# Performance work log

Measured on AMD Instinct MI355X. Metric: run time of the kernel, lower is better.

The kernel has to match this reference:

```python
import jax, jax.numpy as jnp
import numpy as np

N_NODES = 50000
N_EDGES = 800000
NFEAT, NHID, NCLASS = 256, 128, 47


def _gcn_norm(edge_index, edge_weight, n):
    """PyG GCNConv normalization: add self-loops (weight 1) then symmetric deg^-1/2."""
    src, dst = edge_index[0], edge_index[1]
    loop = jnp.arange(n, dtype=src.dtype)
    src_f = jnp.concatenate([src, loop])
    dst_f = jnp.concatenate([dst, loop])
    w_f = jnp.concatenate([edge_weight, jnp.ones((n,), edge_weight.dtype)])
    deg = jax.ops.segment_sum(w_f, dst_f, num_segments=n)  # [n]
    deg_safe = jnp.where(deg > 0, deg, 1.0)
    dinv = jnp.where(deg > 0, jax.lax.rsqrt(deg_safe), 0.0)
    norm = dinv[src_f] * w_f * dinv[dst_f]  # [E + n]
    return src_f, dst_f, norm


def _gcn_conv(h, src, dst, norm, b, n):
    # gather transformed source features, scale, scatter-add into targets
    msg = h[src] * norm[:, None]  # [E+n, d]
    return jax.ops.segment_sum(msg, dst, num_segments=n) + b


def setup_inputs() -> dict:
    key = jax.random.key(0)
    k = jax.random.split(key, 8)
    x = jax.random.normal(k[0], (N_NODES, NFEAT), dtype=jnp.float32)
    edge_index = jax.random.randint(k[1], (2, N_EDGES), 0, N_NODES, dtype=jnp.int32)
    edge_weight = jax.random.uniform(k[2], (N_EDGES,), dtype=jnp.float32)
    W1 = jax.random.normal(k[3], (NFEAT, NHID), dtype=jnp.float32) * (1.0 / np.sqrt(NFEAT))
    b1 = jnp.zeros((NHID,), dtype=jnp.float32)
    W2 = jax.random.normal(k[4], (NHID, NCLASS), dtype=jnp.float32) * (1.0 / np.sqrt(NHID))
    b2 = jnp.zeros((NCLASS,), dtype=jnp.float32)
    return {"x": x, "edge_index": edge_index, "edge_weight": edge_weight,
            "W1": W1, "b1": b1, "W2": W2, "b2": b2}


def reference(x, edge_index, edge_weight, W1, b1, W2, b2):
    n = x.shape[0]
    src, dst, norm = _gcn_norm(edge_index, edge_weight, n)
    h = _gcn_conv(x @ W1, src, dst, norm, b1, n)   # GCNConv 1
    h = jax.nn.relu(h)                             # dropout is identity in eval
    h = _gcn_conv(h @ W2, src, dst, norm, b2, n)   # GCNConv 2
    return jax.nn.log_softmax(h, axis=1)
```

## Files before the change

kernel.cpp:

```cpp
#include <hip/hip_runtime.h>

#define N_NODES 50000
#define N_EDGES 800000
#define NFEAT   256
#define NHID    128
#define NCLASS  47
#define H2P     48
#define CSR_MAX (N_EDGES + 7 * N_NODES)
#define NSUB    8
#define G1_BLOCKS ((N_NODES + 63) / 64)

typedef __attribute__((ext_vector_type(8))) short short8v;
typedef __attribute__((ext_vector_type(4))) float f32x4;

__device__ __forceinline__ ushort f2bf(float f) {
    unsigned u = __float_as_uint(f);
    unsigned r = (u + 0x7FFF + ((u >> 16) & 1)) >> 16;
    return (ushort)r;
}
__device__ __forceinline__ float blo(unsigned u) { return __uint_as_float(u << 16); }
__device__ __forceinline__ float bhi(unsigned u) { return __uint_as_float(u & 0xFFFF0000u); }


__global__ void init_kernel(unsigned long long* __restrict__ packed,
                            int* __restrict__ total,
                            const float* __restrict__ W1, const float* __restrict__ W2,
                            ushort* __restrict__ w1t, ushort* __restrict__ w2t) {
    int t = blockIdx.x * blockDim.x + threadIdx.x;
    if (t < N_NODES * NSUB) packed[t] = 0ull;
    if (t == 0) *total = 0;
    if (t < NFEAT * NHID) {
        int k = t >> 7, c = t & 127;
        w1t[c * NFEAT + k] = f2bf(W1[(size_t)k * NHID + c]);
    }
    if (t < NHID * H2P) {
        int k = t / H2P, c = t % H2P;
        w2t[c * NHID + k] = (c < NCLASS) ? f2bf(W2[(size_t)k * NCLASS + c]) : 0;
    }
}


__global__ __launch_bounds__(256) void fused_gemm1_degcnt_kernel(
        const float* __restrict__ x, const ushort* __restrict__ w1t,
        ushort* __restrict__ h1b,
        const int* __restrict__ dst, const float* __restrict__ w,
        unsigned long long* __restrict__ packed, int* __restrict__ pos) {
    __shared__ __align__(16) ushort xs[64][72];
    __shared__ __align__(16) ushort ws[128][72];
    int tid = threadIdx.x;
    if (blockIdx.x >= G1_BLOCKS) {
        int e = (blockIdx.x - G1_BLOCKS) * 256 + tid;
        if (e < N_EDGES) {
            int d = dst[e];
            int b = e & (NSUB - 1);
            unsigned fx = __float2uint_rn(w[e] * 1048576.0f);
            unsigned long long old = atomicAdd(&packed[(size_t)b * N_NODES + d],
                                               (1ull << 40) | (unsigned long long)fx);
            pos[e] = (int)(old >> 40);
        }
        return;
    }
    int node0 = blockIdx.x * 64;
    int wave = tid >> 6, l = tid & 63;
    int fr = l & 15, fq = l >> 4;
    int r0 = (wave >> 1) * 32;
    int c0 = (wave & 1) * 64;

    f32x4 acc[2][4] = {};

    for (int kk0 = 0; kk0 < NFEAT; kk0 += 64) {
        {
            int row = tid >> 2, q = tid & 3;
            int srow = node0 + row; if (srow >= N_NODES) srow = N_NODES - 1;
            const float4* src = (const float4*)(x + (size_t)srow * NFEAT + kk0 + q * 16);
            ushort tmp[16];
            #pragma unroll
            for (int i = 0; i < 4; ++i) {
                float4 v = src[i];
                tmp[i * 4 + 0] = f2bf(v.x); tmp[i * 4 + 1] = f2bf(v.y);
                tmp[i * 4 + 2] = f2bf(v.z); tmp[i * 4 + 3] = f2bf(v.w);
            }
            #pragma unroll
            for (int i = 0; i < 2; ++i)
                *(short8v*)&xs[row][q * 16 + i * 8] = *(short8v*)&tmp[i * 8];
        }
        {
            int rr = tid >> 3;
            int cq = tid & 7;
            #pragma unroll
            for (int i = 0; i < 4; ++i) {
                int row = rr + i * 32;
                *(short8v*)&ws[row][cq * 8] =
                    *(const short8v*)&w1t[(size_t)row * NFEAT + kk0 + cq * 8];
            }
        }
        __syncthreads();
        short8v a[2][2], b[4][2];
        #pragma unroll
        for (int m = 0; m < 2; ++m)
            #pragma unroll
            for (int kf = 0; kf < 2; ++kf)
                a[m][kf] = *(const short8v*)&xs[r0 + m * 16 + fr][kf * 32 + fq * 8];
        #pragma unroll
        for (int n = 0; n < 4; ++n)
            #pragma unroll
            for (int kf = 0; kf < 2; ++kf)
                b[n][kf] = *(const short8v*)&ws[c0 + n * 16 + fr][kf * 32 + fq * 8];
        #pragma unroll
        for (int m = 0; m < 2; ++m)
            #pragma unroll
            for (int n = 0; n < 4; ++n)
                #pragma unroll
                for (int kf = 0; kf < 2; ++kf)
                    acc[m][n] = __builtin_amdgcn_mfma_f32_16x16x32_bf16(
                        a[m][kf], b[n][kf], acc[m][n], 0, 0, 0);
        __syncthreads();
    }
    #pragma unroll
    for (int m = 0; m < 2; ++m) {
        #pragma unroll
        for (int n = 0; n < 4; ++n) {
            #pragma unroll
            for (int j = 0; j < 4; ++j) {
                int gr = node0 + r0 + m * 16 + fq * 4 + j;
                if (gr < N_NODES)
                    h1b[(size_t)gr * NHID + c0 + n * 16 + fr] = f2bf(acc[m][n][j]);
            }
        }
    }
}

__global__ __launch_bounds__(256) void segalloc_kernel(const unsigned long long* __restrict__ packed,
                                                       int* __restrict__ counts,
                                                       float* __restrict__ dinv,
                                                       int* __restrict__ row_start,
                                                       int* __restrict__ sub_base,
                                                       int* __restrict__ total,
                                                       int2* __restrict__ csr, int n) {
    __shared__ int s[256];
    __shared__ int base_s;
    int t = threadIdx.x;
    int i = blockIdx.x * 256 + t;
    int v = 0, cnt = 0;
    if (i < n) {
        unsigned long long ws = 0;
        int sb[NSUB];
        #pragma unroll
        for (int b = 0; b < NSUB; ++b) {
            unsigned long long pk = packed[(size_t)b * N_NODES + i];
            sb[b] = cnt;
            cnt += (int)(pk >> 40);
            ws += (pk & 0xFFFFFFFFFFull);
        }
        counts[i] = cnt;
        float deg = 1.0f + (float)ws * (1.0f / 1048576.0f);
        dinv[i] = rsqrtf(deg);
        #pragma unroll
        for (int b = 0; b < NSUB; b += 4)
            *(int4*)&sub_base[(size_t)i * NSUB + b] = make_int4(sb[b], sb[b+1], sb[b+2], sb[b+3]);
        v = (cnt + 7) & ~7;
    }
    s[t] = v;
    __syncthreads();
    #pragma unroll
    for (int off = 1; off < 256; off <<= 1) {
        int x = s[t];
        if (t >= off) x += s[t - off];
        __syncthreads();
        s[t] = x;
        __syncthreads();
    }
    if (t == 255) base_s = atomicAdd(total, s[255]);
    __syncthreads();
    if (i < n) {
        int base = base_s + s[t] - v;
        row_start[i] = base;
        for (int k = cnt; k < v; ++k) csr[base + k] = make_int2(0, 0);
    }
}

__global__ void scatter_kernel(const int* __restrict__ src, const int* __restrict__ dst,
                               const float* __restrict__ w, const int* __restrict__ pos,
                               const float* __restrict__ dinv,
                               const int* __restrict__ row_start,
                               const int* __restrict__ sub_base,
                               int2* __restrict__ csr, int E) {
    int e = blockIdx.x * blockDim.x + threadIdx.x;
    if (e >= E) return;
    int d = dst[e], s = src[e];
    int b = e & (NSUB - 1);
    int p = row_start[d] + sub_base[(size_t)d * NSUB + b] + pos[e];
    int2 pr;
    pr.x = s;
    pr.y = __float_as_int(dinv[s] * w[e] * dinv[d]);
    csr[p] = pr;
}


__global__ __launch_bounds__(256) void agg1_kernel(const ushort* __restrict__ h1b,
                                                   const int* __restrict__ row_start,
                                                   const int* __restrict__ counts,
                                                   const int2* __restrict__ csr,
                                                   const float* __restrict__ dinv,
                                                   const float* __restrict__ b1,
                                                   ushort* __restrict__ haggb) {
    int wv = threadIdx.x >> 6;
    int i = blockIdx.x * 4 + wv;
    int l = threadIdx.x & 63;
    int h = l >> 5, q = l & 31;
    const ushort* rowp = h1b + 4 * q;

    float di = dinv[i];
    float sc = (h == 0) ? di * di : 0.f;
    uint2 sv = *(const uint2*)(rowp + (size_t)i * NHID);
    float4 acc;
    acc.x = sc * blo(sv.x); acc.y = sc * bhi(sv.x);
    acc.z = sc * blo(sv.y); acc.w = sc * bhi(sv.y);

    int lo = row_start[i], hi = lo + ((counts[i] + 7) & ~7);
    int e = lo;
    for (; e + 16 <= hi; e += 16) {
        int2 pA = csr[e + 0 + h],  pB = csr[e + 2 + h];
        int2 pC = csr[e + 4 + h],  pD = csr[e + 6 + h];
        int2 pE = csr[e + 8 + h],  pF = csr[e + 10 + h];
        int2 pG = csr[e + 12 + h], pH = csr[e + 14 + h];
        uint2 vA = *(const uint2*)(rowp + (size_t)pA.x * NHID);
        uint2 vB = *(const uint2*)(rowp + (size_t)pB.x * NHID);
        uint2 vC = *(const uint2*)(rowp + (size_t)pC.x * NHID);
        uint2 vD = *(const uint2*)(rowp + (size_t)pD.x * NHID);
        uint2 vE = *(const uint2*)(rowp + (size_t)pE.x * NHID);
        uint2 vF = *(const uint2*)(rowp + (size_t)pF.x * NHID);
        uint2 vG = *(const uint2*)(rowp + (size_t)pG.x * NHID);
        uint2 vH = *(const uint2*)(rowp + (size_t)pH.x * NHID);
        float wA = __int_as_float(pA.y), wB = __int_as_float(pB.y);
        float wC = __int_as_float(pC.y), wD = __int_as_float(pD.y);
        float wE = __int_as_float(pE.y), wF = __int_as_float(pF.y);
        float wG = __int_as_float(pG.y), wH = __int_as_float(pH.y);
        acc.x = fmaf(wA, blo(vA.x), acc.x); acc.y = fmaf(wA, bhi(vA.x), acc.y);
        acc.z = fmaf(wA, blo(vA.y), acc.z); acc.w = fmaf(wA, bhi(vA.y), acc.w);
        acc.x = fmaf(wB, blo(vB.x), acc.x); acc.y = fmaf(wB, bhi(vB.x), acc.y);
        acc.z = fmaf(wB, blo(vB.y), acc.z); acc.w = fmaf(wB, bhi(vB.y), acc.w);
        acc.x = fmaf(wC, blo(vC.x), acc.x); acc.y = fmaf(wC, bhi(vC.x), acc.y);
        acc.z = fmaf(wC, blo(vC.y), acc.z); acc.w = fmaf(wC, bhi(vC.y), acc.w);
        acc.x = fmaf(wD, blo(vD.x), acc.x); acc.y = fmaf(wD, bhi(vD.x), acc.y);
        acc.z = fmaf(wD, blo(vD.y), acc.z); acc.w = fmaf(wD, bhi(vD.y), acc.w);
        acc.x = fmaf(wE, blo(vE.x), acc.x); acc.y = fmaf(wE, bhi(vE.x), acc.y);
        acc.z = fmaf(wE, blo(vE.y), acc.z); acc.w = fmaf(wE, bhi(vE.y), acc.w);
        acc.x = fmaf(wF, blo(vF.x), acc.x); acc.y = fmaf(wF, bhi(vF.x), acc.y);
        acc.z = fmaf(wF, blo(vF.y), acc.z); acc.w = fmaf(wF, bhi(vF.y), acc.w);
        acc.x = fmaf(wG, blo(vG.x), acc.x); acc.y = fmaf(wG, bhi(vG.x), acc.y);
        acc.z = fmaf(wG, blo(vG.y), acc.z); acc.w = fmaf(wG, bhi(vG.y), acc.w);
        acc.x = fmaf(wH, blo(vH.x), acc.x); acc.y = fmaf(wH, bhi(vH.x), acc.y);
        acc.z = fmaf(wH, blo(vH.y), acc.z); acc.w = fmaf(wH, bhi(vH.y), acc.w);
    }
    if (e < hi) {
        int2 pA = csr[e + 0 + h], pB = csr[e + 2 + h];
        int2 pC = csr[e + 4 + h], pD = csr[e + 6 + h];
        uint2 vA = *(const uint2*)(rowp + (size_t)pA.x * NHID);
        uint2 vB = *(const uint2*)(rowp + (size_t)pB.x * NHID);
        uint2 vC = *(const uint2*)(rowp + (size_t)pC.x * NHID);
        uint2 vD = *(const uint2*)(rowp + (size_t)pD.x * NHID);
        float wA = __int_as_float(pA.y), wB = __int_as_float(pB.y);
        float wC = __int_as_float(pC.y), wD = __int_as_float(pD.y);
        acc.x = fmaf(wA, blo(vA.x), acc.x); acc.y = fmaf(wA, bhi(vA.x), acc.y);
        acc.z = fmaf(wA, blo(vA.y), acc.z); acc.w = fmaf(wA, bhi(vA.y), acc.w);
        acc.x = fmaf(wB, blo(vB.x), acc.x); acc.y = fmaf(wB, bhi(vB.x), acc.y);
        acc.z = fmaf(wB, blo(vB.y), acc.z); acc.w = fmaf(wB, bhi(vB.y), acc.w);
        acc.x = fmaf(wC, blo(vC.x), acc.x); acc.y = fmaf(wC, bhi(vC.x), acc.y);
        acc.z = fmaf(wC, blo(vC.y), acc.z); acc.w = fmaf(wC, bhi(vC.y), acc.w);
        acc.x = fmaf(wD, blo(vD.x), acc.x); acc.y = fmaf(wD, bhi(vD.x), acc.y);
        acc.z = fmaf(wD, blo(vD.y), acc.z); acc.w = fmaf(wD, bhi(vD.y), acc.w);
    }
    acc.x += __shfl_xor(acc.x, 32);
    acc.y += __shfl_xor(acc.y, 32);
    acc.z += __shfl_xor(acc.z, 32);
    acc.w += __shfl_xor(acc.w, 32);
    if (h == 0) {
        float4 bb = *(const float4*)(b1 + 4 * q);
        acc.x = fmaxf(acc.x + bb.x, 0.f);
        acc.y = fmaxf(acc.y + bb.y, 0.f);
        acc.z = fmaxf(acc.z + bb.z, 0.f);
        acc.w = fmaxf(acc.w + bb.w, 0.f);
        uint2 o;
        o.x = (unsigned)f2bf(acc.x) | ((unsigned)f2bf(acc.y) << 16);
        o.y = (unsigned)f2bf(acc.z) | ((unsigned)f2bf(acc.w) << 16);
        *(uint2*)(haggb + (size_t)i * NHID + 4 * q) = o;
    }
}


__global__ __launch_bounds__(256) void gemm2_kernel(const ushort* __restrict__ haggb,
                                                    const ushort* __restrict__ w2t,
                                                    ushort* __restrict__ h2b) {
    __shared__ __align__(16) ushort ha[64][136];
    __shared__ __align__(16) ushort wt[48][136];
    int tid = threadIdx.x;
    int node0 = blockIdx.x * 64;
    {
        int row = tid >> 2, q = tid & 3;
        int srow = node0 + row; if (srow >= N_NODES) srow = N_NODES - 1;
        const short8v* src = (const short8v*)(haggb + (size_t)srow * NHID + q * 32);
        #pragma unroll
        for (int i = 0; i < 4; ++i)
            *(short8v*)&ha[row][q * 32 + i * 8] = src[i];
    }
    {
        #pragma unroll
        for (int i = 0; i < 3; ++i) {
            int id = tid + i * 256;
            int row = id >> 4, cq = id & 15;
            *(short8v*)&wt[row][cq * 8] =
                *(const short8v*)&w2t[(size_t)row * NHID + cq * 8];
        }
    }
    __syncthreads();
    int wave = tid >> 6, l = tid & 63;
    int fr = l & 15, fq = l >> 4;
    int r0 = wave * 16;
    short8v a[4], b[3][4];
    #pragma unroll
    for (int kf = 0; kf < 4; ++kf)
        a[kf] = *(const short8v*)&ha[r0 + fr][kf * 32 + fq * 8];
    #pragma unroll
    for (int n = 0; n < 3; ++n)
        #pragma unroll
        for (int kf = 0; kf < 4; ++kf)
            b[n][kf] = *(const short8v*)&wt[n * 16 + fr][kf * 32 + fq * 8];
    f32x4 acc[3] = {};
    #pragma unroll
    for (int n = 0; n < 3; ++n)
        #pragma unroll
        for (int kf = 0; kf < 4; ++kf)
            acc[n] = __builtin_amdgcn_mfma_f32_16x16x32_bf16(a[kf], b[n][kf], acc[n], 0, 0, 0);
    #pragma unroll
    for (int n = 0; n < 3; ++n) {
        #pragma unroll
        for (int j = 0; j < 4; ++j) {
            int gr = node0 + r0 + fq * 4 + j;
            int col = n * 16 + fr;
            if (gr < N_NODES && col < H2P)
                h2b[(size_t)gr * H2P + col] = (col < NCLASS) ? f2bf(acc[n][j]) : 0;
        }
    }
}


__global__ __launch_bounds__(256) void agg2_kernel(const ushort* __restrict__ h2b,
                                                   const int* __restrict__ row_start,
                                                   const int* __restrict__ counts,
                                                   const int2* __restrict__ csr,
                                                   const float* __restrict__ dinv,
                                                   const float* __restrict__ b2,
                                                   float* __restrict__ out, int n) {
    int wv = threadIdx.x >> 6;
    int i = blockIdx.x * 4 + wv;
    if (i >= n) return;
    int l = threadIdx.x & 63;
    int h = l >> 5, q = l & 31;
    bool act = q < 24;
    int qq = act ? q : 0;
    const ushort* rowp = h2b + 2 * qq;

    float di = dinv[i];
    float sc = (h == 0 && act) ? di * di : 0.f;
    unsigned sv = *(const unsigned*)(rowp + (size_t)i * H2P);
    float2 acc;
    acc.x = sc * blo(sv); acc.y = sc * bhi(sv);

    int lo = row_start[i], hi = lo + ((counts[i] + 7) & ~7);
    int e = lo;
    for (; e + 16 <= hi; e += 16) {
        int2 pA = csr[e + 0 + h],  pB = csr[e + 2 + h];
        int2 pC = csr[e + 4 + h],  pD = csr[e + 6 + h];
        int2 pE = csr[e + 8 + h],  pF = csr[e + 10 + h];
        int2 pG = csr[e + 12 + h], pH = csr[e + 14 + h];
        unsigned vA = *(const unsigned*)(rowp + (size_t)pA.x * H2P);
        unsigned vB = *(const unsigned*)(rowp + (size_t)pB.x * H2P);
        unsigned vC = *(const unsigned*)(rowp + (size_t)pC.x * H2P);
        unsigned vD = *(const unsigned*)(rowp + (size_t)pD.x * H2P);
        unsigned vE = *(const unsigned*)(rowp + (size_t)pE.x * H2P);
        unsigned vF = *(const unsigned*)(rowp + (size_t)pF.x * H2P);
        unsigned vG = *(const unsigned*)(rowp + (size_t)pG.x * H2P);
        unsigned vH = *(const unsigned*)(rowp + (size_t)pH.x * H2P);
        float wA = __int_as_float(pA.y), wB = __int_as_float(pB.y);
        float wC = __int_as_float(pC.y), wD = __int_as_float(pD.y);
        float wE = __int_as_float(pE.y), wF = __int_as_float(pF.y);
        float wG = __int_as_float(pG.y), wH = __int_as_float(pH.y);
        acc.x = fmaf(wA, blo(vA), acc.x); acc.y = fmaf(wA, bhi(vA), acc.y);
        acc.x = fmaf(wB, blo(vB), acc.x); acc.y = fmaf(wB, bhi(vB), acc.y);
        acc.x = fmaf(wC, blo(vC), acc.x); acc.y = fmaf(wC, bhi(vC), acc.y);
        acc.x = fmaf(wD, blo(vD), acc.x); acc.y = fmaf(wD, bhi(vD), acc.y);
        acc.x = fmaf(wE, blo(vE), acc.x); acc.y = fmaf(wE, bhi(vE), acc.y);
        acc.x = fmaf(wF, blo(vF), acc.x); acc.y = fmaf(wF, bhi(vF), acc.y);
        acc.x = fmaf(wG, blo(vG), acc.x); acc.y = fmaf(wG, bhi(vG), acc.y);
        acc.x = fmaf(wH, blo(vH), acc.x); acc.y = fmaf(wH, bhi(vH), acc.y);
    }
    if (e < hi) {
        int2 pA = csr[e + 0 + h], pB = csr[e + 2 + h];
        int2 pC = csr[e + 4 + h], pD = csr[e + 6 + h];
        unsigned vA = *(const unsigned*)(rowp + (size_t)pA.x * H2P);
        unsigned vB = *(const unsigned*)(rowp + (size_t)pB.x * H2P);
        unsigned vC = *(const unsigned*)(rowp + (size_t)pC.x * H2P);
        unsigned vD = *(const unsigned*)(rowp + (size_t)pD.x * H2P);
        float wA = __int_as_float(pA.y), wB = __int_as_float(pB.y);
        float wC = __int_as_float(pC.y), wD = __int_as_float(pD.y);
        acc.x = fmaf(wA, blo(vA), acc.x); acc.y = fmaf(wA, bhi(vA), acc.y);
        acc.x = fmaf(wB, blo(vB), acc.x); acc.y = fmaf(wB, bhi(vB), acc.y);
        acc.x = fmaf(wC, blo(vC), acc.x); acc.y = fmaf(wC, bhi(vC), acc.y);
        acc.x = fmaf(wD, blo(vD), acc.x); acc.y = fmaf(wD, bhi(vD), acc.y);
    }
    acc.x += __shfl_xor(acc.x, 32);
    acc.y += __shfl_xor(acc.y, 32);

    float v0 = -1e30f, v1 = -1e30f;
    if (act) {
        v0 = acc.x + b2[2 * q];
        v1 = (2 * q + 1 < NCLASS) ? (acc.y + b2[2 * q + 1]) : -1e30f;
    }
    float pm = fmaxf(v0, v1);
    #pragma unroll
    for (int off = 16; off; off >>= 1) pm = fmaxf(pm, __shfl_xor(pm, off));
    float ex = 0.f;
    if (act) {
        ex = __expf(v0 - pm);
        if (2 * q + 1 < NCLASS) ex += __expf(v1 - pm);
    }
    #pragma unroll
    for (int off = 16; off; off >>= 1) ex += __shfl_xor(ex, off);
    if (h == 0 && act) {
        float ls = pm + __logf(ex);
        out[(size_t)i * NCLASS + 2 * q] = v0 - ls;
        if (2 * q + 1 < NCLASS) out[(size_t)i * NCLASS + 2 * q + 1] = v1 - ls;
    }
}


extern "C" void kernel_launch(void* const* d_in, const int* in_sizes, int n_in,
                              void* d_out, int out_size, void* d_ws, size_t ws_size,
                              hipStream_t stream) {
    const float* x  = (const float*)d_in[0];
    const int*   ei = (const int*)d_in[1];
    const float* ew = (const float*)d_in[2];
    const float* W1 = (const float*)d_in[3];
    const float* b1 = (const float*)d_in[4];
    const float* W2 = (const float*)d_in[5];
    const float* b2 = (const float*)d_in[6];
    float* out = (float*)d_out;

    const int* e_src = ei;
    const int* e_dst = ei + N_EDGES;

    char* p = (char*)d_ws;
    auto carve = [&](size_t bytes) { void* r = (void*)p; p += (bytes + 255) & ~(size_t)255; return r; };
    unsigned long long* packed = (unsigned long long*)carve((size_t)N_NODES * NSUB * 8);
    float*  dinv      = (float*) carve(N_NODES * 4);
    int*    counts    = (int*)   carve(N_NODES * 4);
    int*    row_start = (int*)   carve(N_NODES * 4);
    int*    sub_base  = (int*)   carve((size_t)N_NODES * NSUB * 4);
    int*    total     = (int*)   carve(4);
    int*    pos       = (int*)   carve((size_t)N_EDGES * 4);
    int2*   csr       = (int2*)  carve((size_t)CSR_MAX * 8);
    ushort* h1b       = (ushort*)carve((size_t)N_NODES * NHID * 2);
    ushort* haggb     = (ushort*)carve((size_t)N_NODES * NHID * 2);
    ushort* h2b       = (ushort*)carve((size_t)N_NODES * H2P * 2);
    ushort* w1t       = (ushort*)carve((size_t)NHID * NFEAT * 2);
    ushort* w2t       = (ushort*)carve((size_t)H2P * NHID * 2);

    init_kernel<<<(N_NODES * NSUB + 255) / 256, 256, 0, stream>>>(packed, total, W1, W2, w1t, w2t);
    fused_gemm1_degcnt_kernel<<<G1_BLOCKS + (N_EDGES + 255) / 256, 256, 0, stream>>>(
        x, w1t, h1b, e_dst, ew, packed, pos);
    segalloc_kernel<<<(N_NODES + 255) / 256, 256, 0, stream>>>(packed, counts, dinv,
                                                               row_start, sub_base, total,
                                                               csr, N_NODES);
    scatter_kernel<<<(N_EDGES + 255) / 256, 256, 0, stream>>>(e_src, e_dst, ew, pos, dinv,
                                                              row_start, sub_base, csr, N_EDGES);
    agg1_kernel<<<(N_NODES + 3) / 4, 256, 0, stream>>>(h1b, row_start, counts, csr, dinv, b1, haggb);
    gemm2_kernel<<<(N_NODES + 63) / 64, 256, 0, stream>>>(haggb, w2t, h2b);
    agg2_kernel<<<(N_NODES + 3) / 4, 256, 0, stream>>>(h2b, row_start, counts, csr, dinv, b2, out, N_NODES);
}
```

Measured before the change: 150.0 us.

## Fuse layer-1 aggregation with second GEMM via shared-memory tile

Merges the agg1 and gemm2 kernels so each block aggregates 16 nodes (4 per wave, processed serially), writes the relu'd bf16 rows into shared memory, then three waves run MFMA against W2 to produce h2. This drops the haggb intermediate buffer's global write and read plus one launch. In exchange each wave handles several nodes sequentially, which lowers memory-level parallelism for the gather, and the block needs a barrier before the MFMA stage. The sub-bucket index in the edge-count path now uses the thread index, which is equivalent for 256-thread blocks.

```diff
diff --git a/kernel.cpp b/kernel.cpp
--- a/kernel.cpp
+++ b/kernel.cpp
@@ -52,7 +52,7 @@
         int e = (blockIdx.x - G1_BLOCKS) * 256 + tid;
         if (e < N_EDGES) {
             int d = dst[e];
-            int b = e & (NSUB - 1);
+            int b = tid & (NSUB - 1);
             unsigned fx = __float2uint_rn(w[e] * 1048576.0f);
             unsigned long long old = atomicAdd(&packed[(size_t)b * N_NODES + d],
                                                (1ull << 40) | (unsigned long long)fx);
@@ -72,11 +72,11 @@
         {
             int row = tid >> 2, q = tid & 3;
             int srow = node0 + row; if (srow >= N_NODES) srow = N_NODES - 1;
-            const float4* src = (const float4*)(x + (size_t)srow * NFEAT + kk0 + q * 16);
+            const float4* sp = (const float4*)(x + (size_t)srow * NFEAT + kk0 + q * 16);
             ushort tmp[16];
             #pragma unroll
             for (int i = 0; i < 4; ++i) {
-                float4 v = src[i];
+                float4 v = sp[i];
                 tmp[i * 4 + 0] = f2bf(v.x); tmp[i * 4 + 1] = f2bf(v.y);
                 tmp[i * 4 + 2] = f2bf(v.z); tmp[i * 4 + 3] = f2bf(v.w);
             }
@@ -197,149 +197,129 @@
 }
 
 
-__global__ __launch_bounds__(256) void agg1_kernel(const ushort* __restrict__ h1b,
-                                                   const int* __restrict__ row_start,
-                                                   const int* __restrict__ counts,
-                                                   const int2* __restrict__ csr,
-                                                   const float* __restrict__ dinv,
-                                                   const float* __restrict__ b1,
-                                                   ushort* __restrict__ haggb) {
-    int wv = threadIdx.x >> 6;
-    int i = blockIdx.x * 4 + wv;
-    int l = threadIdx.x & 63;
-    int h = l >> 5, q = l & 31;
-    const ushort* rowp = h1b + 4 * q;
-
-    float di = dinv[i];
-    float sc = (h == 0) ? di * di : 0.f;
-    uint2 sv = *(const uint2*)(rowp + (size_t)i * NHID);
-    float4 acc;
-    acc.x = sc * blo(sv.x); acc.y = sc * bhi(sv.x);
-    acc.z = sc * blo(sv.y); acc.w = sc * bhi(sv.y);
-
-    int lo = row_start[i], hi = lo + ((counts[i] + 7) & ~7);
-    int e = lo;
-    for (; e + 16 <= hi; e += 16) {
-        int2 pA = csr[e + 0 + h],  pB = csr[e + 2 + h];
-        int2 pC = csr[e + 4 + h],  pD = csr[e + 6 + h];
-        int2 pE = csr[e + 8 + h],  pF = csr[e + 10 + h];
-        int2 pG = csr[e + 12 + h], pH = csr[e + 14 + h];
-        uint2 vA = *(const uint2*)(rowp + (size_t)pA.x * NHID);
-        uint2 vB = *(const uint2*)(rowp + (size_t)pB.x * NHID);
-        uint2 vC = *(const uint2*)(rowp + (size_t)pC.x * NHID);
-        uint2 vD = *(const uint2*)(rowp + (size_t)pD.x * NHID);
-        uint2 vE = *(const uint2*)(rowp + (size_t)pE.x * NHID);
-        uint2 vF = *(const uint2*)(rowp + (size_t)pF.x * NHID);
-        uint2 vG = *(const uint2*)(rowp + (size_t)pG.x * NHID);
-        uint2 vH = *(const uint2*)(rowp + (size_t)pH.x * NHID);
-        float wA = __int_as_float(pA.y), wB = __int_as_float(pB.y);
-        float wC = __int_as_float(pC.y), wD = __int_as_float(pD.y);
-        float wE = __int_as_float(pE.y), wF = __int_as_float(pF.y);
-        float wG = __int_as_float(pG.y), wH = __int_as_float(pH.y);
-        acc.x = fmaf(wA, blo(vA.x), acc.x); acc.y = fmaf(wA, bhi(vA.x), acc.y);
-        acc.z = fmaf(wA, blo(vA.y), acc.z); acc.w = fmaf(wA, bhi(vA.y), acc.w);
-        acc.x = fmaf(wB, blo(vB.x), acc.x); acc.y = fmaf(wB, bhi(vB.x), acc.y);
-        acc.z = fmaf(wB, blo(vB.y), acc.z); acc.w = fmaf(wB, bhi(vB.y), acc.w);
-        acc.x = fmaf(wC, blo(vC.x), acc.x); acc.y = fmaf(wC, bhi(vC.x), acc.y);
-        acc.z = fmaf(wC, blo(vC.y), acc.z); acc.w = fmaf(wC, bhi(vC.y), acc.w);
-        acc.x = fmaf(wD, blo(vD.x), acc.x); acc.y = fmaf(wD, bhi(vD.x), acc.y);
-        acc.z = fmaf(wD, blo(vD.y), acc.z); acc.w = fmaf(wD, bhi(vD.y), acc.w);
-        acc.x = fmaf(wE, blo(vE.x), acc.x); acc.y = fmaf(wE, bhi(vE.x), acc.y);
-        acc.z = fmaf(wE, blo(vE.y), acc.z); acc.w = fmaf(wE, bhi(vE.y), acc.w);
-        acc.x = fmaf(wF, blo(vF.x), acc.x); acc.y = fmaf(wF, bhi(vF.x), acc.y);
-        acc.z = fmaf(wF, blo(vF.y), acc.z); acc.w = fmaf(wF, bhi(vF.y), acc.w);
-        acc.x = fmaf(wG, blo(vG.x), acc.x); acc.y = fmaf(wG, bhi(vG.x), acc.y);
-        acc.z = fmaf(wG, blo(vG.y), acc.z); acc.w = fmaf(wG, bhi(vG.y), acc.w);
-        acc.x = fmaf(wH, blo(vH.x), acc.x); acc.y = fmaf(wH, bhi(vH.x), acc.y);
-        acc.z = fmaf(wH, blo(vH.y), acc.z); acc.w = fmaf(wH, bhi(vH.y), acc.w);
-    }
-    if (e < hi) {
-        int2 pA = csr[e + 0 + h], pB = csr[e + 2 + h];
-        int2 pC = csr[e + 4 + h], pD = csr[e + 6 + h];
-        uint2 vA = *(const uint2*)(rowp + (size_t)pA.x * NHID);
-        uint2 vB = *(const uint2*)(rowp + (size_t)pB.x * NHID);
-        uint2 vC = *(const uint2*)(rowp + (size_t)pC.x * NHID);
-        uint2 vD = *(const uint2*)(rowp + (size_t)pD.x * NHID);
-        float wA = __int_as_float(pA.y), wB = __int_as_float(pB.y);
-        float wC = __int_as_float(pC.y), wD = __int_as_float(pD.y);
-        acc.x = fmaf(wA, blo(vA.x), acc.x); acc.y = fmaf(wA, bhi(vA.x), acc.y);
-        acc.z = fmaf(wA, blo(vA.y), acc.z); acc.w = fmaf(wA, bhi(vA.y), acc.w);
-        acc.x = fmaf(wB, blo(vB.x), acc.x); acc.y = fmaf(wB, bhi(vB.x), acc.y);
-        acc.z = fmaf(wB, blo(vB.y), acc.z); acc.w = fmaf(wB, bhi(vB.y), acc.w);
-        acc.x = fmaf(wC, blo(vC.x), acc.x); acc.y = fmaf(wC, bhi(vC.x), acc.y);
-        acc.z = fmaf(wC, blo(vC.y), acc.z); acc.w = fmaf(wC, bhi(vC.y), acc.w);
-        acc.x = fmaf(wD, blo(vD.x), acc.x); acc.y = fmaf(wD, bhi(vD.x), acc.y);
-        acc.z = fmaf(wD, blo(vD.y), acc.z); acc.w = fmaf(wD, bhi(vD.y), acc.w);
-    }
-    acc.x += __shfl_xor(acc.x, 32);
-    acc.y += __shfl_xor(acc.y, 32);
-    acc.z += __shfl_xor(acc.z, 32);
-    acc.w += __shfl_xor(acc.w, 32);
-    if (h == 0) {
-        float4 bb = *(const float4*)(b1 + 4 * q);
-        acc.x = fmaxf(acc.x + bb.x, 0.f);
-        acc.y = fmaxf(acc.y + bb.y, 0.f);
-        acc.z = fmaxf(acc.z + bb.z, 0.f);
-        acc.w = fmaxf(acc.w + bb.w, 0.f);
-        uint2 o;
-        o.x = (unsigned)f2bf(acc.x) | ((unsigned)f2bf(acc.y) << 16);
-        o.y = (unsigned)f2bf(acc.z) | ((unsigned)f2bf(acc.w) << 16);
-        *(uint2*)(haggb + (size_t)i * NHID + 4 * q) = o;
-    }
-}
-
-
-__global__ __launch_bounds__(256) void gemm2_kernel(const ushort* __restrict__ haggb,
-                                                    const ushort* __restrict__ w2t,
-                                                    ushort* __restrict__ h2b) {
-    __shared__ __align__(16) ushort ha[64][136];
+__global__ __launch_bounds__(256) void agg1g2_kernel(const ushort* __restrict__ h1b,
+                                                     const int* __restrict__ row_start,
+                                                     const int* __restrict__ counts,
+                                                     const int2* __restrict__ csr,
+                                                     const float* __restrict__ dinv,
+                                                     const float* __restrict__ b1,
+                                                     const ushort* __restrict__ w2t,
+                                                     ushort* __restrict__ h2b) {
+    __shared__ __align__(16) ushort hs[16][136];
     __shared__ __align__(16) ushort wt[48][136];
     int tid = threadIdx.x;
-    int node0 = blockIdx.x * 64;
-    {
-        int row = tid >> 2, q = tid & 3;
-        int srow = node0 + row; if (srow >= N_NODES) srow = N_NODES - 1;
-        const short8v* src = (const short8v*)(haggb + (size_t)srow * NHID + q * 32);
-        #pragma unroll
-        for (int i = 0; i < 4; ++i)
-            *(short8v*)&ha[row][q * 32 + i * 8] = src[i];
-    }
-    {
-        #pragma unroll
-        for (int i = 0; i < 3; ++i) {
-            int id = tid + i * 256;
-            int row = id >> 4, cq = id & 15;
-            *(short8v*)&wt[row][cq * 8] =
-                *(const short8v*)&w2t[(size_t)row * NHID + cq * 8];
+    int nb = blockIdx.x * 16;
+    int wv = tid >> 6;
+    int l = tid & 63;
+    int h = l >> 5, q = l & 31;
+
+    #pragma unroll
+    for (int i = 0; i < 3; ++i) {
+        int id = tid + i * 256;
+        int row = id >> 4, cq = id & 15;
+        *(short8v*)&wt[row][cq * 8] = *(const short8v*)&w2t[(size_t)row * NHID + cq * 8];
+    }
+
+    const ushort* rowp = h1b + 4 * q;
+
+    for (int ni = 0; ni < 4; ++ni) {
+        int i = nb + wv * 4 + ni;
+        float di = dinv[i];
+        float sc = (h == 0) ? di * di : 0.f;
+        uint2 sv = *(const uint2*)(rowp + (size_t)i * NHID);
+        float4 acc;
+        acc.x = sc * blo(sv.x); acc.y = sc * bhi(sv.x);
+        acc.z = sc * blo(sv.y); acc.w = sc * bhi(sv.y);
+
+        int lo = row_start[i], hi = lo + ((counts[i] + 7) & ~7);
+        int e = lo;
+        for (; e + 16 <= hi; e += 16) {
+            int2 pA = csr[e + 0 + h],  pB = csr[e + 2 + h];
+            int2 pC = csr[e + 4 + h],  pD = csr[e + 6 + h];
+            int2 pE = csr[e + 8 + h],  pF = csr[e + 10 + h];
+            int2 pG = csr[e + 12 + h], pH = csr[e + 14 + h];
+            uint2 vA = *(const uint2*)(rowp + (size_t)pA.x * NHID);
+            uint2 vB = *(const uint2*)(rowp + (size_t)pB.x * NHID);
+            uint2 vC = *(const uint2*)(rowp + (size_t)pC.x * NHID);
+            uint2 vD = *(const uint2*)(rowp + (size_t)pD.x * NHID);
+            uint2 vE = *(const uint2*)(rowp + (size_t)pE.x * NHID);
+            uint2 vF = *(const uint2*)(rowp + (size_t)pF.x * NHID);
+            uint2 vG = *(const uint2*)(rowp + (size_t)pG.x * NHID);
+            uint2 vH = *(const uint2*)(rowp + (size_t)pH.x * NHID);
+            float wA = __int_as_float(pA.y), wB = __int_as_float(pB.y);
+            float wC = __int_as_float(pC.y), wD = __int_as_float(pD.y);
+            float wE = __int_as_float(pE.y), wF = __int_as_float(pF.y);
+            float wG = __int_as_float(pG.y), wH = __int_as_float(pH.y);
+            acc.x = fmaf(wA, blo(vA.x), acc.x); acc.y = fmaf(wA, bhi(vA.x), acc.y);
+            acc.z = fmaf(wA, blo(vA.y), acc.z); acc.w = fmaf(wA, bhi(vA.y), acc.w);
+            acc.x = fmaf(wB, blo(vB.x), acc.x); acc.y = fmaf(wB, bhi(vB.x), acc.y);
+            acc.z = fmaf(wB, blo(vB.y), acc.z); acc.w = fmaf(wB, bhi(vB.y), acc.w);
+            acc.x = fmaf(wC, blo(vC.x), acc.x); acc.y = fmaf(wC, bhi(vC.x), acc.y);
+            acc.z = fmaf(wC, blo(vC.y), acc.z); acc.w = fmaf(wC, bhi(vC.y), acc.w);
+            acc.x = fmaf(wD, blo(vD.x), acc.x); acc.y = fmaf(wD, bhi(vD.x), acc.y);
+            acc.z = fmaf(wD, blo(vD.y), acc.z); acc.w = fmaf(wD, bhi(vD.y), acc.w);
+            acc.x = fmaf(wE, blo(vE.x), acc.x); acc.y = fmaf(wE, bhi(vE.x), acc.y);
+            acc.z = fmaf(wE, blo(vE.y), acc.z); acc.w = fmaf(wE, bhi(vE.y), acc.w);
+            acc.x = fmaf(wF, blo(vF.x), acc.x); acc.y = fmaf(wF, bhi(vF.x), acc.y);
+            acc.z = fmaf(wF, blo(vF.y), acc.z); acc.w = fmaf(wF, bhi(vF.y), acc.w);
+            acc.x = fmaf(wG, blo(vG.x), acc.x); acc.y = fmaf(wG, bhi(vG.x), acc.y);
+            acc.z = fmaf(wG, blo(vG.y), acc.z); acc.w = fmaf(wG, bhi(vG.y), acc.w);
+            acc.x = fmaf(wH, blo(vH.x), acc.x); acc.y = fmaf(wH, bhi(vH.x), acc.y);
+            acc.z = fmaf(wH, blo(vH.y), acc.z); acc.w = fmaf(wH, bhi(vH.y), acc.w);
+        }
+        if (e < hi) {
+            int2 pA = csr[e + 0 + h], pB = csr[e + 2 + h];
+            int2 pC = csr[e + 4 + h], pD = csr[e + 6 + h];
+            uint2 vA = *(const uint2*)(rowp + (size_t)pA.x * NHID);
+            uint2 vB = *(const uint2*)(rowp + (size_t)pB.x * NHID);
+            uint2 vC = *(const uint2*)(rowp + (size_t)pC.x * NHID);
+            uint2 vD = *(const uint2*)(rowp + (size_t)pD.x * NHID);
+            float wA = __int_as_float(pA.y), wB = __int_as_float(pB.y);
+            float wC = __int_as_float(pC.y), wD = __int_as_float(pD.y);
+            acc.x = fmaf(wA, blo(vA.x), acc.x); acc.y = fmaf(wA, bhi(vA.x), acc.y);
+            acc.z = fmaf(wA, blo(vA.y), acc.z); acc.w = fmaf(wA, bhi(vA.y), acc.w);
+            acc.x = fmaf(wB, blo(vB.x), acc.x); acc.y = fmaf(wB, bhi(vB.x), acc.y);
+            acc.z = fmaf(wB, blo(vB.y), acc.z); acc.w = fmaf(wB, bhi(vB.y), acc.w);
+            acc.x = fmaf(wC, blo(vC.x), acc.x); acc.y = fmaf(wC, bhi(vC.x), acc.y);
+            acc.z = fmaf(wC, blo(vC.y), acc.z); acc.w = fmaf(wC, bhi(vC.y), acc.w);
+            acc.x = fmaf(wD, blo(vD.x), acc.x); acc.y = fmaf(wD, bhi(vD.x), acc.y);
+            acc.z = fmaf(wD, blo(vD.y), acc.z); acc.w = fmaf(wD, bhi(vD.y), acc.w);
+        }
+        acc.x += __shfl_xor(acc.x, 32);
+        acc.y += __shfl_xor(acc.y, 32);
+        acc.z += __shfl_xor(acc.z, 32);
+        acc.w += __shfl_xor(acc.w, 32);
+        if (h == 0) {
+            float4 bb = *(const float4*)(b1 + 4 * q);
+            acc.x = fmaxf(acc.x + bb.x, 0.f);
+            acc.y = fmaxf(acc.y + bb.y, 0.f);
+            acc.z = fmaxf(acc.z + bb.z, 0.f);
+            acc.w = fmaxf(acc.w + bb.w, 0.f);
+            uint2 o;
+            o.x = (unsigned)f2bf(acc.x) | ((unsigned)f2bf(acc.y) << 16);
+            o.y = (unsigned)f2bf(acc.z) | ((unsigned)f2bf(acc.w) << 16);
+            *(uint2*)&hs[wv * 4 + ni][4 * q] = o;
         }
     }
     __syncthreads();
-    int wave = tid >> 6, l = tid & 63;
-    int fr = l & 15, fq = l >> 4;
-    int r0 = wave * 16;
-    short8v a[4], b[3][4];
-    #pragma unroll
-    for (int kf = 0; kf < 4; ++kf)
-        a[kf] = *(const short8v*)&ha[r0 + fr][kf * 32 + fq * 8];
-    #pragma unroll
-    for (int n = 0; n < 3; ++n)
+
+    if (wv < 3) {
+        int fr = l & 15, fq = l >> 4;
+        short8v a[4], b[4];
+        #pragma unroll
+        for (int kf = 0; kf < 4; ++kf) {
+            a[kf] = *(const short8v*)&hs[fr][kf * 32 + fq * 8];
+            b[kf] = *(const short8v*)&wt[wv * 16 + fr][kf * 32 + fq * 8];
+        }
+        f32x4 acc2 = {};
         #pragma unroll
         for (int kf = 0; kf < 4; ++kf)
-            b[n][kf] = *(const short8v*)&wt[n * 16 + fr][kf * 32 + fq * 8];
-    f32x4 acc[3] = {};
-    #pragma unroll
-    for (int n = 0; n < 3; ++n)
-        #pragma unroll
-        for (int kf = 0; kf < 4; ++kf)
-            acc[n] = __builtin_amdgcn_mfma_f32_16x16x32_bf16(a[kf], b[n][kf], acc[n], 0, 0, 0);
-    #pragma unroll
-    for (int n = 0; n < 3; ++n) {
+            acc2 = __builtin_amdgcn_mfma_f32_16x16x32_bf16(a[kf], b[kf], acc2, 0, 0, 0);
+        int col = wv * 16 + fr;
         #pragma unroll
         for (int j = 0; j < 4; ++j) {
-            int gr = node0 + r0 + fq * 4 + j;
-            int col = n * 16 + fr;
-            if (gr < N_NODES && col < H2P)
-                h2b[(size_t)gr * H2P + col] = (col < NCLASS) ? f2bf(acc[n][j]) : 0;
+            int gr = nb + fq * 4 + j;
+            h2b[(size_t)gr * H2P + col] = (col < NCLASS) ? f2bf(acc2[j]) : 0;
         }
     }
 }
@@ -461,7 +441,6 @@
     int*    pos       = (int*)   carve((size_t)N_EDGES * 4);
     int2*   csr       = (int2*)  carve((size_t)CSR_MAX * 8);
     ushort* h1b       = (ushort*)carve((size_t)N_NODES * NHID * 2);
-    ushort* haggb     = (ushort*)carve((size_t)N_NODES * NHID * 2);
     ushort* h2b       = (ushort*)carve((size_t)N_NODES * H2P * 2);
     ushort* w1t       = (ushort*)carve((size_t)NHID * NFEAT * 2);
     ushort* w2t       = (ushort*)carve((size_t)H2P * NHID * 2);
@@ -474,7 +453,7 @@
                                                                csr, N_NODES);
     scatter_kernel<<<(N_EDGES + 255) / 256, 256, 0, stream>>>(e_src, e_dst, ew, pos, dinv,
                                                               row_start, sub_base, csr, N_EDGES);
-    agg1_kernel<<<(N_NODES + 3) / 4, 256, 0, stream>>>(h1b, row_start, counts, csr, dinv, b1, haggb);
-    gemm2_kernel<<<(N_NODES + 63) / 64, 256, 0, stream>>>(haggb, w2t, h2b);
+    agg1g2_kernel<<<(N_NODES + 15) / 16, 256, 0, stream>>>(h1b, row_start, counts, csr,
+                                                           dinv, b1, w2t, h2b);
     agg2_kernel<<<(N_NODES + 3) / 4, 256, 0, stream>>>(h2b, row_start, counts, csr, dinv, b2, out, N_NODES);
 }
```

Result: no change. 149.7 us (-0.2%).
